# Kernel tuning notes

Hardware: AMD Instinct MI355X
Metric: run time of the kernel (lower is better)

## Reference

```python
import jax, jax.numpy as jnp
import numpy as np

TAU = 2.0        # LIF membrane time constant
VTH = 1.0        # firing threshold
ALPHA = 4.0      # surrogate sigmoid sharpness
BN_EPS = 1e-5

@jax.custom_vjp
def heaviside_surrogate(x):
    # Forward: hard threshold. Backward: sigmoid surrogate gradient (alpha=4).
    return (x >= 0.0).astype(x.dtype)

def _hs_fwd(x):
    return heaviside_surrogate(x), x

def _hs_bwd(x, g):
    s = jax.nn.sigmoid(ALPHA * x)
    return (g * ALPHA * s * (1.0 - s),)

heaviside_surrogate.defvjp(_hs_fwd, _hs_bwd)


def setup_inputs() -> dict:
    key = jax.random.key(0)
    k1, k2 = jax.random.split(key)
    B, Cin, T, Cout = 64, 512, 1024, 256
    x = jax.random.normal(k1, (B, Cin, T), dtype=jnp.float32)
    W = jax.random.normal(k2, (Cout, Cin), dtype=jnp.float32) * (1.0 / np.sqrt(Cin))
    gamma = jnp.ones((Cout,), dtype=jnp.float32)
    beta = jnp.zeros((Cout,), dtype=jnp.float32)
    run_mean = jnp.zeros((Cout,), dtype=jnp.float32)
    run_var = jnp.ones((Cout,), dtype=jnp.float32)
    return {"x": x, "W": W, "gamma": gamma, "beta": beta,
            "run_mean": run_mean, "run_var": run_var}


def reference(x, W, gamma, beta, run_mean, run_var):
    # Dropout is identity in eval mode.
    # conv1d, kernel_size=1, no bias -> pointwise GEMM over channels: [B,Cin,T] -> [B,Cout,T]
    y = jnp.einsum('bct,oc->bot', x, W)
    # BatchNorm1d (inference, running stats), per-channel affine
    inv = jax.lax.rsqrt(run_var + BN_EPS)
    y = (y - run_mean[None, :, None]) * (inv * gamma)[None, :, None] + beta[None, :, None]
    # LIF recurrence over the time dim (last axis), hard reset to 0, detach_reset.
    yt = jnp.transpose(y, (2, 0, 1))  # [T, B, Cout]

    def step(v, x_t):
        v = v + (x_t - v) / TAU              # decay_input charge
        s = heaviside_surrogate(v - VTH)     # spike via surrogate threshold
        v = v * (1.0 - jax.lax.stop_gradient(s))  # hard reset (detached)
        return v, s

    v0 = jnp.zeros(yt.shape[1:], dtype=yt.dtype)
    _, spikes = jax.lax.scan(step, v0, yt)   # spikes: [T, B, Cout]
    # out.mean(dim=-1) == spike rate over time
    return spikes.mean(axis=0)               # [B, Cout]
```

## Files before the change

### kernel.cpp

```cpp
#include <hip/hip_runtime.h>
#include <math.h>

typedef _Float16 f16;
typedef __attribute__((ext_vector_type(8)))  _Float16 f16v8;
typedef __attribute__((ext_vector_type(4)))  __fp16   h16v4;
typedef __attribute__((ext_vector_type(16))) float    f32x16;
typedef __attribute__((ext_vector_type(4)))  float    f32x4;

namespace {
constexpr int kB = 64, kCin = 512, kT = 1024, kCout = 256;
constexpr size_t kYBytes     = (size_t)kB * kT * kCout * 4;
constexpr size_t kWfragBytes = (size_t)32 * 8 * 2 * 64 * 16;
constexpr size_t kSBytes     = kCout * 4;
constexpr size_t kWsNeed     = kYBytes + kWfragBytes + kSBytes;
}

__global__ void wsplit16_kernel(const float* __restrict__ W, const float* __restrict__ gamma,
                                const float* __restrict__ rvar,
                                f16* __restrict__ wfrag, float* __restrict__ sarr) {
    const int kc = blockIdx.x, osub = blockIdx.y, p = blockIdx.z;
    const int lane = threadIdx.x;
    const int o  = osub * 32 + (lane & 31);
    const int kb = kc * 16 + (lane >> 5) * 8;
    f16v8 frag;
#pragma unroll
    for (int j = 0; j < 8; ++j) {
        const float w = 32.0f * W[o * kCin + kb + j];
        const f16 h = (f16)w;
        const float r = w - (float)h;
        const f16 l = (f16)(r * 2048.0f);
        frag[j] = p ? l : h;
    }
    *reinterpret_cast<f16v8*>(wfrag + ((size_t)((kc * 8 + osub) * 2 + p) * 64 + lane) * 8) = frag;
    if (kc == 0 && osub == 0 && p == 0) {
#pragma unroll
        for (int j = 0; j < 4; ++j) {
            const int oo = j * 64 + lane;
            sarr[oo] = (float)((double)gamma[oo] / sqrt((double)rvar[oo] + 1e-5));
        }
    }
}

__global__ __launch_bounds__(512, 2)
void gemm_f16_kernel(const float* __restrict__ x, const f16* __restrict__ wfrag,
                     const float* __restrict__ sarr, const float* __restrict__ rmean,
                     const float* __restrict__ beta, float* __restrict__ yt) {
    __shared__ unsigned int Bd[4][128 * 20];

    const int tid  = threadIdx.x;
    const int lane = tid & 63;
    const int wave = tid >> 6;
    const int n = lane & 31, q = lane >> 5;
    const int b   = blockIdx.y;
    const int tg0 = blockIdx.x * 128;
    const int osg = wave;
    const float* __restrict__ xb = x + ((size_t)b << 19);
    const f16v8* __restrict__ wf = reinterpret_cast<const f16v8*>(wfrag);

    const int st_t = tid & 127;
    const int kpp  = tid >> 7;
    const int st_sw = (st_t >> 3) & 3;
    const int wr_base = 20 * st_t + 2 * (kpp & 1);
    const int s0 = ((0 + (kpp >> 1)) ^ st_sw) * 4;
    const int s1 = ((2 + (kpp >> 1)) ^ st_sw) * 4;

    f32x16 accA[4] = {};
    f32x16 accB[4] = {};
    f16v8  af[2][2];
    float  xq[4][4];

    auto loadX = [&](int kc, float (&xd)[4]) {
        const float* px = xb + (size_t)(kc * 16 + 4 * kpp) * kT + tg0 + st_t;
#pragma unroll
        for (int r = 0; r < 4; ++r) xd[r] = px[(size_t)r * kT];
    };
    auto loadA = [&](int kc, f16v8 (&ad)[2]) {
#pragma unroll
        for (int pp = 0; pp < 2; ++pp)
            ad[pp] = wf[(size_t)((kc * 8 + osg) * 2 + pp) * 64 + lane];
    };
    auto stage = [&](int buf, const float (&xd)[4]) {
        auto h01 = __builtin_amdgcn_cvt_pkrtz(xd[0], xd[1]);
        auto h23 = __builtin_amdgcn_cvt_pkrtz(xd[2], xd[3]);
        auto l01 = __builtin_amdgcn_cvt_pkrtz((xd[0] - (float)h01[0]) * 2048.0f,
                                              (xd[1] - (float)h01[1]) * 2048.0f);
        auto l23 = __builtin_amdgcn_cvt_pkrtz((xd[2] - (float)h23[0]) * 2048.0f,
                                              (xd[3] - (float)h23[1]) * 2048.0f);
        h16v4 hv, lv;
        hv[0] = h01[0]; hv[1] = h01[1]; hv[2] = h23[0]; hv[3] = h23[1];
        lv[0] = l01[0]; lv[1] = l01[1]; lv[2] = l23[0]; lv[3] = l23[1];
        *reinterpret_cast<h16v4*>(&Bd[buf][wr_base + s0]) = hv;
        *reinterpret_cast<h16v4*>(&Bd[buf][wr_base + s1]) = lv;
    };
    auto domfma = [&](int buf, const f16v8 (&ad)[2]) {
        __builtin_amdgcn_s_setprio(1);
#pragma unroll
        for (int s = 0; s < 4; ++s) {
            const int t = s * 32 + n;
            const int sw = (t >> 3) & 3;
            const f16v8 bh = *reinterpret_cast<const f16v8*>(&Bd[buf][20 * t + 4 * ((0 + q) ^ sw)]);
            const f16v8 bl = *reinterpret_cast<const f16v8*>(&Bd[buf][20 * t + 4 * ((2 + q) ^ sw)]);
            accA[s] = __builtin_amdgcn_mfma_f32_32x32x16_f16(ad[0], bh, accA[s], 0, 0, 0);
            accB[s] = __builtin_amdgcn_mfma_f32_32x32x16_f16(ad[0], bl, accB[s], 0, 0, 0);
            accB[s] = __builtin_amdgcn_mfma_f32_32x32x16_f16(ad[1], bh, accB[s], 0, 0, 0);
        }
        __builtin_amdgcn_s_setprio(0);
    };

    loadX(0, xq[0]); loadX(1, xq[1]); loadX(2, xq[2]); loadX(3, xq[3]);
    loadA(0, af[0]);
    stage(0, xq[0]);
    stage(1, xq[1]);
    asm volatile("s_waitcnt lgkmcnt(0)\n\ts_barrier" ::: "memory");

    for (int kc4 = 0; kc4 < 8; ++kc4) {
#pragma unroll
        for (int u = 0; u < 4; ++u) {
            const int kc = kc4 * 4 + u;
            if (kc < 31) loadA(kc + 1, af[(u + 1) & 1]);
            if (kc < 30) stage((u + 2) & 3, xq[(u + 2) & 3]);
            if (kc < 28) loadX(kc + 4, xq[u]);
            domfma(u, af[u & 1]);
            if (u & 1)
                asm volatile("s_waitcnt lgkmcnt(0)\n\ts_barrier" ::: "memory");
        }
    }

#pragma unroll
    for (int s = 0; s < 4; ++s) {
        const f32x16 v = accA[s] + accB[s] * 4.8828125e-4f;
        const size_t t = (size_t)tg0 + s * 32 + n;
#pragma unroll
        for (int g = 0; g < 4; ++g) {
            const int og = osg * 32 + g * 8 + q * 4;
            const f32x4 sv = *reinterpret_cast<const f32x4*>(sarr + og);
            const f32x4 mv = *reinterpret_cast<const f32x4*>(rmean + og);
            const f32x4 bv = *reinterpret_cast<const f32x4*>(beta + og);
#pragma unroll
            for (int r2 = 0; r2 < 4; ++r2) {
                const int o = og + r2;
                const float val = (v[4 * g + r2] * 0.03125f - mv[r2]) * sv[r2] + bv[r2];
                yt[(((size_t)b << 8) + (size_t)o) * 1024 + t] = val;
            }
        }
    }
}

__global__ __launch_bounds__(64)
void lif_kernel(const float* __restrict__ yt, float* __restrict__ out) {
    const int b = blockIdx.x >> 2;
    const int o = ((blockIdx.x & 3) << 6) + threadIdx.x;
    const f32x4* __restrict__ row =
        reinterpret_cast<const f32x4*>(yt) + (((size_t)b << 8) + (size_t)o) * 256;
    float v = 0.f;
    int cnt = 0;
    f32x4 qb[16];
#pragma unroll
    for (int u = 0; u < 16; ++u) qb[u] = row[u];
    for (int jj = 0; jj < 15; ++jj) {
#pragma unroll
        for (int u = 0; u < 16; ++u) {
            const f32x4 cv = qb[u];
            qb[u] = row[jj * 16 + u + 16];
#pragma unroll
            for (int e = 0; e < 4; ++e) {
                v = v + (cv[e] - v) * 0.5f;
                if (v - 1.0f >= 0.0f) { ++cnt; v = 0.f; }
            }
        }
    }
#pragma unroll
    for (int u = 0; u < 16; ++u) {
        const f32x4 cv = qb[u];
#pragma unroll
        for (int e = 0; e < 4; ++e) {
            v = v + (cv[e] - v) * 0.5f;
            if (v - 1.0f >= 0.0f) { ++cnt; v = 0.f; }
        }
    }
    out[((size_t)b << 8) + o] = (float)cnt * (1.0f / 1024.0f);
}

namespace fb {
constexpr int kOTile = 32, kTTile = 128, kCc = 64;
constexpr int kNtt = kT / kTTile, kNcc = kCin / kCc, kYPad = 132;
}

__global__ void wt_transpose_kernel(const float* __restrict__ W, float* __restrict__ Wt) {
    int idx = blockIdx.x * 256 + threadIdx.x;
    int c = idx >> 8, o = idx & 255;
    Wt[idx] = W[o * kCin + c];
}

__global__ __launch_bounds__(256, 2)
void snn_fused_kernel(const float* __restrict__ x, const float* __restrict__ Wt,
                      const float* __restrict__ gamma, const float* __restrict__ beta,
                      const float* __restrict__ rmean, const float* __restrict__ rvar,
                      float* __restrict__ out) {
    using namespace fb;
    __shared__ float xs[kCc][kTTile];
    __shared__ float ws[kCc][kOTile];
    __shared__ float ytile[kOTile][kYPad];
    __shared__ float sarr[kOTile], barr[kOTile], marr[kOTile], vstate[kOTile];
    __shared__ int scnt[kOTile];
    const int tid = threadIdx.x, tx = tid & 31, ty = tid >> 5;
    const int b = blockIdx.y, o_blk = blockIdx.x * kOTile;
    if (tid < kOTile) {
        const int o = o_blk + tid;
        const double dinv = 1.0 / sqrt((double)rvar[o] + 1e-5);
        sarr[tid] = (float)(dinv * (double)gamma[o]);
        barr[tid] = beta[o]; marr[tid] = rmean[o];
        vstate[tid] = 0.0f; scnt[tid] = 0;
    }
    __syncthreads();
    const float* xb = x + (size_t)b * kCin * kT;
    for (int tt = 0; tt < kNtt; ++tt) {
        float acc[4][4];
#pragma unroll
        for (int i = 0; i < 4; ++i)
#pragma unroll
            for (int j = 0; j < 4; ++j) acc[i][j] = 0.0f;
        const int t0 = tt * kTTile;
        for (int cc = 0; cc < kNcc; ++cc) {
#pragma unroll
            for (int k = 0; k < 8; ++k) {
                const int f = tid + 256 * k;
                const int c = f >> 5, tq = f & 31;
                *reinterpret_cast<float4*>(&xs[c][tq * 4]) = *reinterpret_cast<const float4*>(
                    xb + (size_t)(cc * kCc + c) * kT + t0 + tq * 4);
            }
#pragma unroll
            for (int k = 0; k < 2; ++k) {
                const int f = tid + 256 * k;
                const int c = f >> 3, oq = f & 7;
                *reinterpret_cast<float4*>(&ws[c][oq * 4]) = *reinterpret_cast<const float4*>(
                    Wt + (size_t)(cc * kCc + c) * kCout + o_blk + oq * 4);
            }
            __syncthreads();
#pragma unroll 8
            for (int c = 0; c < kCc; ++c) {
                const float4 xv = *reinterpret_cast<const float4*>(&xs[c][tx * 4]);
                const float4 wv = *reinterpret_cast<const float4*>(&ws[c][ty * 4]);
                const float xf[4] = {xv.x, xv.y, xv.z, xv.w};
                const float wf4[4] = {wv.x, wv.y, wv.z, wv.w};
#pragma unroll
                for (int i = 0; i < 4; ++i)
#pragma unroll
                    for (int j = 0; j < 4; ++j) acc[i][j] += wf4[i] * xf[j];
            }
            __syncthreads();
        }
#pragma unroll
        for (int i = 0; i < 4; ++i) {
            const int o = ty * 4 + i;
            const float s = sarr[o], bb2 = barr[o], m = marr[o];
#pragma unroll
            for (int j = 0; j < 4; ++j) ytile[o][tx * 4 + j] = (acc[i][j] - m) * s + bb2;
        }
        __syncthreads();
        if (tid < kOTile) {
            float vv = vstate[tid];
            int cnt = 0;
#pragma unroll 4
            for (int t = 0; t < kTTile; ++t) {
                const float yv = ytile[tid][t];
                vv = vv + (yv - vv) * 0.5f;
                if (vv - 1.0f >= 0.0f) { cnt++; vv = 0.0f; }
            }
            vstate[tid] = vv; scnt[tid] += cnt;
        }
        __syncthreads();
    }
    if (tid < kOTile) out[b * kCout + o_blk + tid] = (float)scnt[tid] * (1.0f / 1024.0f);
}

extern "C" void kernel_launch(void* const* d_in, const int* in_sizes, int n_in,
                              void* d_out, int out_size, void* d_ws, size_t ws_size,
                              hipStream_t stream) {
    const float* x     = (const float*)d_in[0];
    const float* W     = (const float*)d_in[1];
    const float* gamma = (const float*)d_in[2];
    const float* beta  = (const float*)d_in[3];
    const float* rmean = (const float*)d_in[4];
    const float* rvar  = (const float*)d_in[5];
    float* out = (float*)d_out;

    if (ws_size >= kWsNeed) {
        float* yt    = (float*)d_ws;
        f16*   wfrag = (f16*)((char*)d_ws + kYBytes);
        float* sarr  = (float*)((char*)d_ws + kYBytes + kWfragBytes);
        wsplit16_kernel<<<dim3(32, 8, 2), 64, 0, stream>>>(W, gamma, rvar, wfrag, sarr);
        gemm_f16_kernel<<<dim3(8, 64), 512, 0, stream>>>(x, wfrag, sarr, rmean, beta, yt);
        lif_kernel<<<256, 64, 0, stream>>>(yt, out);
    } else {
        float* Wt = (float*)d_ws;
        wt_transpose_kernel<<<(kCin * kCout) / 256, 256, 0, stream>>>(W, Wt);
        snn_fused_kernel<<<dim3(kCout / fb::kOTile, kB), 256, 0, stream>>>(
            x, Wt, gamma, beta, rmean, rvar, out);
    }
}
```

Before: 244.3 us.

## Fuse LIF recurrence into GEMM kernel, drop the global y intermediate

The GEMM and LIF kernels are merged. Each block now owns one batch and a 64-channel quarter and walks all 1024 timesteps in 8 chunks of 128. After each chunk it writes the BN-scaled tile to LDS, and 64 threads advance the membrane state serially. This removes the 64 MB write and read-back of the y intermediate and one kernel launch. The cost is that each block now redoes the x staging for every quarter, so x is loaded four times as often, and the serial LIF phase idles most waves between chunks.

```diff
diff --git a/kernel.cpp b/kernel.cpp
--- a/kernel.cpp
+++ b/kernel.cpp
@@ -9,10 +9,9 @@
 
 namespace {
 constexpr int kB = 64, kCin = 512, kT = 1024, kCout = 256;
-constexpr size_t kYBytes     = (size_t)kB * kT * kCout * 4;
 constexpr size_t kWfragBytes = (size_t)32 * 8 * 2 * 64 * 16;
 constexpr size_t kSBytes     = kCout * 4;
-constexpr size_t kWsNeed     = kYBytes + kWfragBytes + kSBytes;
+constexpr size_t kWsNeed     = kWfragBytes + kSBytes;
 }
 
 __global__ void wsplit16_kernel(const float* __restrict__ W, const float* __restrict__ gamma,
@@ -42,18 +41,24 @@
 }
 
 __global__ __launch_bounds__(512, 2)
-void gemm_f16_kernel(const float* __restrict__ x, const f16* __restrict__ wfrag,
-                     const float* __restrict__ sarr, const float* __restrict__ rmean,
-                     const float* __restrict__ beta, float* __restrict__ yt) {
+void gemmlif_kernel(const float* __restrict__ x, const f16* __restrict__ wfrag,
+                    const float* __restrict__ sarr, const float* __restrict__ rmean,
+                    const float* __restrict__ beta, float* __restrict__ out) {
     __shared__ unsigned int Bd[4][128 * 20];
+    __shared__ float ytile[64][132];
 
     const int tid  = threadIdx.x;
     const int lane = tid & 63;
     const int wave = tid >> 6;
     const int n = lane & 31, q = lane >> 5;
-    const int b   = blockIdx.y;
-    const int tg0 = blockIdx.x * 128;
-    const int osg = wave;
+
+    const int bid     = blockIdx.x;
+    const int r       = bid >> 3;
+    const int quarter = r & 3;
+    const int b       = (bid & 7) + 8 * (r >> 2);
+    const int osub_loc = wave & 1;
+    const int tsub     = wave >> 1;
+    const int osg      = quarter * 2 + osub_loc;
     const float* __restrict__ xb = x + ((size_t)b << 19);
     const f16v8* __restrict__ wf = reinterpret_cast<const f16v8*>(wfrag);
 
@@ -64,16 +69,21 @@
     const int s0 = ((0 + (kpp >> 1)) ^ st_sw) * 4;
     const int s1 = ((2 + (kpp >> 1)) ^ st_sw) * 4;
 
-    f32x16 accA[4] = {};
-    f32x16 accB[4] = {};
-    f16v8  af[2][2];
-    float  xq[4][4];
-
-    auto loadX = [&](int kc, float (&xd)[4]) {
-        const float* px = xb + (size_t)(kc * 16 + 4 * kpp) * kT + tg0 + st_t;
-#pragma unroll
-        for (int r = 0; r < 4; ++r) xd[r] = px[(size_t)r * kT];
-    };
+    f32x4 sv[4], mv[4], bv[4];
+#pragma unroll
+    for (int g = 0; g < 4; ++g) {
+        const int og = osg * 32 + g * 8 + q * 4;
+        sv[g] = *reinterpret_cast<const f32x4*>(sarr + og);
+        mv[g] = *reinterpret_cast<const f32x4*>(rmean + og);
+        bv[g] = *reinterpret_cast<const f32x4*>(beta + og);
+    }
+
+    float vv = 0.0f;
+    int   cnt = 0;
+
+    f16v8 af[2][2];
+    float xq[4][4];
+
     auto loadA = [&](int kc, f16v8 (&ad)[2]) {
 #pragma unroll
         for (int pp = 0; pp < 2; ++pp)
@@ -92,93 +102,90 @@
         *reinterpret_cast<h16v4*>(&Bd[buf][wr_base + s0]) = hv;
         *reinterpret_cast<h16v4*>(&Bd[buf][wr_base + s1]) = lv;
     };
-    auto domfma = [&](int buf, const f16v8 (&ad)[2]) {
-        __builtin_amdgcn_s_setprio(1);
-#pragma unroll
-        for (int s = 0; s < 4; ++s) {
-            const int t = s * 32 + n;
+
+    for (int tc = 0; tc < 8; ++tc) {
+        const int tg0 = tc * 128;
+        f32x16 accA = {};
+        f32x16 accB = {};
+
+        auto loadX = [&](int kc, float (&xd)[4]) {
+            const float* px = xb + (size_t)(kc * 16 + 4 * kpp) * kT + tg0 + st_t;
+#pragma unroll
+            for (int rr = 0; rr < 4; ++rr) xd[rr] = px[(size_t)rr * kT];
+        };
+        auto domfma = [&](int buf, const f16v8 (&ad)[2]) {
+            __builtin_amdgcn_s_setprio(1);
+            const int t = tsub * 32 + n;
             const int sw = (t >> 3) & 3;
             const f16v8 bh = *reinterpret_cast<const f16v8*>(&Bd[buf][20 * t + 4 * ((0 + q) ^ sw)]);
             const f16v8 bl = *reinterpret_cast<const f16v8*>(&Bd[buf][20 * t + 4 * ((2 + q) ^ sw)]);
-            accA[s] = __builtin_amdgcn_mfma_f32_32x32x16_f16(ad[0], bh, accA[s], 0, 0, 0);
-            accB[s] = __builtin_amdgcn_mfma_f32_32x32x16_f16(ad[0], bl, accB[s], 0, 0, 0);
-            accB[s] = __builtin_amdgcn_mfma_f32_32x32x16_f16(ad[1], bh, accB[s], 0, 0, 0);
-        }
-        __builtin_amdgcn_s_setprio(0);
-    };
-
-    loadX(0, xq[0]); loadX(1, xq[1]); loadX(2, xq[2]); loadX(3, xq[3]);
-    loadA(0, af[0]);
-    stage(0, xq[0]);
-    stage(1, xq[1]);
-    asm volatile("s_waitcnt lgkmcnt(0)\n\ts_barrier" ::: "memory");
-
-    for (int kc4 = 0; kc4 < 8; ++kc4) {
-#pragma unroll
-        for (int u = 0; u < 4; ++u) {
-            const int kc = kc4 * 4 + u;
-            if (kc < 31) loadA(kc + 1, af[(u + 1) & 1]);
-            if (kc < 30) stage((u + 2) & 3, xq[(u + 2) & 3]);
-            if (kc < 28) loadX(kc + 4, xq[u]);
-            domfma(u, af[u & 1]);
-            if (u & 1)
-                asm volatile("s_waitcnt lgkmcnt(0)\n\ts_barrier" ::: "memory");
-        }
-    }
-
-#pragma unroll
-    for (int s = 0; s < 4; ++s) {
-        const f32x16 v = accA[s] + accB[s] * 4.8828125e-4f;
-        const size_t t = (size_t)tg0 + s * 32 + n;
-#pragma unroll
-        for (int g = 0; g < 4; ++g) {
-            const int og = osg * 32 + g * 8 + q * 4;
-            const f32x4 sv = *reinterpret_cast<const f32x4*>(sarr + og);
-            const f32x4 mv = *reinterpret_cast<const f32x4*>(rmean + og);
-            const f32x4 bv = *reinterpret_cast<const f32x4*>(beta + og);
-#pragma unroll
-            for (int r2 = 0; r2 < 4; ++r2) {
-                const int o = og + r2;
-                const float val = (v[4 * g + r2] * 0.03125f - mv[r2]) * sv[r2] + bv[r2];
-                yt[(((size_t)b << 8) + (size_t)o) * 1024 + t] = val;
-            }
-        }
-    }
-}
-
-__global__ __launch_bounds__(64)
-void lif_kernel(const float* __restrict__ yt, float* __restrict__ out) {
-    const int b = blockIdx.x >> 2;
-    const int o = ((blockIdx.x & 3) << 6) + threadIdx.x;
-    const f32x4* __restrict__ row =
-        reinterpret_cast<const f32x4*>(yt) + (((size_t)b << 8) + (size_t)o) * 256;
-    float v = 0.f;
-    int cnt = 0;
-    f32x4 qb[16];
-#pragma unroll
-    for (int u = 0; u < 16; ++u) qb[u] = row[u];
-    for (int jj = 0; jj < 15; ++jj) {
-#pragma unroll
-        for (int u = 0; u < 16; ++u) {
-            const f32x4 cv = qb[u];
-            qb[u] = row[jj * 16 + u + 16];
-#pragma unroll
-            for (int e = 0; e < 4; ++e) {
-                v = v + (cv[e] - v) * 0.5f;
-                if (v - 1.0f >= 0.0f) { ++cnt; v = 0.f; }
-            }
-        }
-    }
-#pragma unroll
-    for (int u = 0; u < 16; ++u) {
-        const f32x4 cv = qb[u];
-#pragma unroll
-        for (int e = 0; e < 4; ++e) {
-            v = v + (cv[e] - v) * 0.5f;
-            if (v - 1.0f >= 0.0f) { ++cnt; v = 0.f; }
-        }
-    }
-    out[((size_t)b << 8) + o] = (float)cnt * (1.0f / 1024.0f);
+            accA = __builtin_amdgcn_mfma_f32_32x32x16_f16(ad[0], bh, accA, 0, 0, 0);
+            accB = __builtin_amdgcn_mfma_f32_32x32x16_f16(ad[0], bl, accB, 0, 0, 0);
+            accB = __builtin_amdgcn_mfma_f32_32x32x16_f16(ad[1], bh, accB, 0, 0, 0);
+            __builtin_amdgcn_s_setprio(0);
+        };
+
+        loadX(0, xq[0]); loadX(1, xq[1]); loadX(2, xq[2]); loadX(3, xq[3]);
+        loadA(0, af[0]);
+        stage(0, xq[0]);
+        stage(1, xq[1]);
+        asm volatile("s_waitcnt lgkmcnt(0)\n\ts_barrier" ::: "memory");
+
+        for (int kc4 = 0; kc4 < 8; ++kc4) {
+#pragma unroll
+            for (int u = 0; u < 4; ++u) {
+                const int kc = kc4 * 4 + u;
+                if (kc < 31) loadA(kc + 1, af[(u + 1) & 1]);
+                if (kc < 30) stage((u + 2) & 3, xq[(u + 2) & 3]);
+                if (kc < 28) loadX(kc + 4, xq[u]);
+                domfma(u, af[u & 1]);
+                if (u & 1)
+                    asm volatile("s_waitcnt lgkmcnt(0)\n\ts_barrier" ::: "memory");
+            }
+        }
+
+        {
+            const f32x16 v = accA + accB * 4.8828125e-4f;
+            const int t_loc = tsub * 32 + n;
+#pragma unroll
+            for (int g = 0; g < 4; ++g)
+#pragma unroll
+                for (int r2 = 0; r2 < 4; ++r2) {
+                    const int o_loc = osub_loc * 32 + g * 8 + q * 4 + r2;
+                    const float val = (v[4 * g + r2] * 0.03125f - mv[g][r2]) * sv[g][r2] + bv[g][r2];
+                    ytile[o_loc][t_loc] = val;
+                }
+        }
+        asm volatile("s_waitcnt lgkmcnt(0)\n\ts_barrier" ::: "memory");
+
+        if (tid < 64) {
+            const float* yrow = &ytile[tid][0];
+            f32x4 pA[4], pB[4];
+#pragma unroll
+            for (int j = 0; j < 4; ++j) pA[j] = *reinterpret_cast<const f32x4*>(yrow + j * 4);
+#pragma unroll
+            for (int g = 0; g < 8; ++g) {
+                f32x4* curp = (g & 1) ? pB : pA;
+                f32x4* nxtp = (g & 1) ? pA : pB;
+                if (g < 7) {
+#pragma unroll
+                    for (int j = 0; j < 4; ++j)
+                        nxtp[j] = *reinterpret_cast<const f32x4*>(yrow + (g + 1) * 16 + j * 4);
+                }
+#pragma unroll
+                for (int j = 0; j < 4; ++j)
+#pragma unroll
+                    for (int e = 0; e < 4; ++e) {
+                        const float yv = curp[j][e];
+                        vv = vv + (yv - vv) * 0.5f;
+                        if (vv - 1.0f >= 0.0f) { ++cnt; vv = 0.0f; }
+                    }
+            }
+        }
+    }
+
+    if (tid < 64)
+        out[((size_t)b << 8) + (quarter << 6) + tid] = (float)cnt * (1.0f / 1024.0f);
 }
 
 namespace fb {
@@ -259,15 +266,15 @@
         }
         __syncthreads();
         if (tid < kOTile) {
-            float vv = vstate[tid];
-            int cnt = 0;
+            float vvv = vstate[tid];
+            int cnt2 = 0;
 #pragma unroll 4
             for (int t = 0; t < kTTile; ++t) {
                 const float yv = ytile[tid][t];
-                vv = vv + (yv - vv) * 0.5f;
-                if (vv - 1.0f >= 0.0f) { cnt++; vv = 0.0f; }
-            }
-            vstate[tid] = vv; scnt[tid] += cnt;
+                vvv = vvv + (yv - vvv) * 0.5f;
+                if (vvv - 1.0f >= 0.0f) { cnt2++; vvv = 0.0f; }
+            }
+            vstate[tid] = vvv; scnt[tid] += cnt2;
         }
         __syncthreads();
     }
@@ -286,12 +293,10 @@
     float* out = (float*)d_out;
 
     if (ws_size >= kWsNeed) {
-        float* yt    = (float*)d_ws;
-        f16*   wfrag = (f16*)((char*)d_ws + kYBytes);
-        float* sarr  = (float*)((char*)d_ws + kYBytes + kWfragBytes);
+        f16*   wfrag = (f16*)d_ws;
+        float* sarr  = (float*)((char*)d_ws + kWfragBytes);
         wsplit16_kernel<<<dim3(32, 8, 2), 64, 0, stream>>>(W, gamma, rvar, wfrag, sarr);
-        gemm_f16_kernel<<<dim3(8, 64), 512, 0, stream>>>(x, wfrag, sarr, rmean, beta, yt);
-        lif_kernel<<<256, 64, 0, stream>>>(yt, out);
+        gemmlif_kernel<<<dim3(256), 512, 0, stream>>>(x, wfrag, sarr, rmean, beta, out);
     } else {
         float* Wt = (float*)d_ws;
         wt_transpose_kernel<<<(kCin * kCout) / 256, 256, 0, stream>>>(W, Wt);
```

New measurement: 273.2 us. 1.12x slower.
